# Kernel optimization log

Measured on AMD Instinct MI355X. Metric: run time of the kernel, lower is better.

Reference implementation:

```python
import jax, jax.numpy as jnp
import numpy as np

GAMMA = 0.5      # temperature from __init__
SOS_ID = 2       # constant <sos> token id
EPS = 1e-10


def setup_inputs() -> dict:
    key = jax.random.key(0)
    ks = jax.random.split(key, 12)
    B, T, E, DY, DZ, V = 64, 32, 100, 200, 500, 32000
    H = DY + DZ
    s = lambda k, shape, sc=1.0: (jax.random.normal(k, shape, jnp.float32) * sc)
    return {
        "z": s(ks[0], (B, DZ), 0.1),
        "labels": jax.random.uniform(ks[1], (B,), jnp.float32),
        "W_fc": s(ks[2], (DY, 1), 0.1),
        "b_fc": s(ks[3], (DY,), 0.1),
        "embed_weight": s(ks[4], (V, E), 0.1),
        "W_ih": s(ks[5], (3 * H, E), 0.05),
        "W_hh": s(ks[6], (3 * H, H), 0.05),
        "b_ih": s(ks[7], (3 * H,), 0.05),
        "b_hh": s(ks[8], (3 * H,), 0.05),
        "W_out": s(ks[9], (V, H), 0.05),
        "b_out": s(ks[10], (V,), 0.05),
        "gumbel_u": jax.random.uniform(ks[11], (T - 1, B, V), jnp.float32),
        "src": jax.random.randint(jax.random.fold_in(key, 99), (T, B), 0, V),
        "src_len": T,
    }


def _gru_step(h, x, W_ih, W_hh, b_ih, b_hh):
    # PyTorch GRU cell: gates ordered (r, z, n)
    gi = x @ W_ih.T + b_ih          # [B, 3H]
    gh = h @ W_hh.T + b_hh          # [B, 3H]
    i_r, i_z, i_n = jnp.split(gi, 3, axis=-1)
    h_r, h_z, h_n = jnp.split(gh, 3, axis=-1)
    r = jax.nn.sigmoid(i_r + h_r)
    zt = jax.nn.sigmoid(i_z + h_z)
    n = jnp.tanh(i_n + r * h_n)
    return (1.0 - zt) * n + zt * h


def reference(z, labels, W_fc, b_fc, embed_weight, W_ih, W_hh, b_ih, b_hh,
              W_out, b_out, gumbel_u, src, src_len):
    B, H = z.shape[0], W_hh.shape[1]
    V = W_out.shape[0]
    # h0 = cat(fc(1 - labels), z)
    h0 = jnp.concatenate([(1.0 - labels)[:, None] @ W_fc.T + b_fc, z], axis=-1)  # [B, H]
    x0 = jnp.broadcast_to(embed_weight[SOS_ID], (B, embed_weight.shape[1]))      # [B, E]

    def step(carry, u):
        h, x = carry
        h = _gru_step(h, x, W_ih, W_hh, b_ih, b_hh)      # [B, H]
        pred = h @ W_out.T + b_out                        # [B, V]
        g = -jnp.log(-jnp.log(u + EPS) + EPS)             # gumbel noise
        y = jax.nn.softmax(pred + g, axis=-1)             # gumbel_softmax, tau=1
        x_next = (y / GAMMA) @ embed_weight               # soft embedding [B, E]
        return (h, x_next), (h, pred)

    (_, _), (outs, preds) = jax.lax.scan(step, (h0, x0), gumbel_u)  # [T-1,B,H], [T-1,B,V]

    dt = z.dtype
    outputs = jnp.concatenate(
        [h0[None], jnp.zeros((1, B, H), dt), outs], axis=0)         # [T+1, B, H]
    predictions = jnp.concatenate(
        [jnp.zeros((1, B, V), dt), preds], axis=0)                  # [T, B, V]
    return outputs, predictions
```

## Files before the change

### kernel.cpp

```cpp
#include <hip/hip_runtime.h>

#define B 64
#define TS 31
#define E 100
#define DY 200
#define DZ 500
#define V 32000
#define H 700
#define HP 704
#define H3 2100
#define XH 800
#define SOS 2
#define OUT_PRED_OFF (33*B*H)
#define NPB 500
#define VCH 125
#define NVCH 256
#define SOFF 15.0f

typedef unsigned short u16;
typedef __attribute__((ext_vector_type(8))) short short8;
typedef __attribute__((ext_vector_type(4))) float f32x4;

__device__ __forceinline__ float sigm(float x) { return 1.f / (1.f + __expf(-x)); }
__device__ __forceinline__ u16 f2b(float f) {
  union { float f; unsigned int u; } c; c.f = f;
  unsigned int u = c.u;
  u16 h = (u16)(u >> 16);
  unsigned int rem = u & 0xFFFFu;
  h += (u16)((rem > 0x8000u) || (rem == 0x8000u && (h & 1)));
  return h;
}

__global__ __launch_bounds__(256) void k_zero(float* __restrict__ out, long n) {
  long i0 = (long)blockIdx.x * 256 + threadIdx.x;
  long st = (long)gridDim.x * 256;
  for (long i = i0; i < n; i += st) out[i] = 0.f;
}

__global__ __launch_bounds__(256) void k0_init(
    const float* __restrict__ z, const float* __restrict__ labels,
    const float* __restrict__ W_fc, const float* __restrict__ b_fc,
    const float* __restrict__ embed, const float* __restrict__ W_ih,
    const float* __restrict__ W_hh, const float* __restrict__ W_out,
    float* __restrict__ out, float* __restrict__ hA, float* __restrict__ WT,
    u16* __restrict__ W2, u16* __restrict__ h_bf,
    float* __restrict__ xacc, float* __restrict__ Z)
{
  long i0 = (long)blockIdx.x * 256 + threadIdx.x;
  long st = (long)gridDim.x * 256;
  if (i0 < B) Z[i0] = 2.f;
  for (long i = i0; i < (long)B * V; i += st) out[OUT_PRED_OFF + i] = 0.f;
  for (long i = i0; i < (long)B * H; i += st) out[B * H + i] = 0.f;
  for (long i = i0; i < (long)B * H; i += st) {
    int b = (int)(i / H), j = (int)(i % H);
    float v = (j < DY) ? (1.f - labels[b]) * W_fc[j] + b_fc[j]
                       : z[b * DZ + (j - DY)];
    hA[i] = v;
    out[i] = v;
  }
  for (long i = i0; i < (long)B * E; i += st) {
    int e = (int)(i % E);
    xacc[i] = embed[SOS * E + e];
  }
  for (long i = i0; i < (long)B * HP; i += st) h_bf[i] = 0;
  for (long i = i0; i < (long)XH * H3; i += st) {
    int k = (int)(i / H3), g = (int)(i % H3);
    WT[i] = (k < E) ? W_ih[(long)g * E + k] : W_hh[(long)g * H + (k - E)];
  }
  for (long i = i0; i < (long)V * HP; i += st) {
    long s8 = i >> 3; int j = (int)(i & 7);
    int lane = (int)(s8 & 63);
    long tmp = s8 >> 6;
    int kk = (int)(tmp % 22);
    long cgrp = tmp / 22;
    int col = (int)(cgrp * 16 + (lane & 15));
    int k = kk * 32 + ((lane >> 4) << 3) + j;
    W2[i] = (k < H) ? f2b(W_out[(size_t)col * H + k]) : (u16)0;
  }
}

__global__ __launch_bounds__(256) void k1a(
    const float* __restrict__ xacc, const float* __restrict__ Z,
    const float* __restrict__ hin, const float* __restrict__ WT,
    const float* __restrict__ b_ih,
    float* __restrict__ gig, float* __restrict__ ghg_p)
{
  int nt = blockIdx.x, c = blockIdx.y;
  int n = nt * 64 + (threadIdx.x & 63);
  int bq = threadIdx.x >> 6;
  __shared__ float xs[64][100];
  __shared__ float invZ[64];
  if (threadIdx.x < 64) invZ[threadIdx.x] = 2.f / Z[threadIdx.x];
  __syncthreads();
  for (int i = threadIdx.x; i < 6400; i += 256) {
    int b = i / 100, kk = i % 100;
    xs[b][kk] = (c == 0) ? xacc[i] * invZ[b] : hin[b * H + (c - 1) * 100 + kk];
  }
  __syncthreads();
  if (n >= H3) return;
  float acc[16];
  #pragma unroll
  for (int bb = 0; bb < 16; ++bb) acc[bb] = 0.f;
  for (int kk = 0; kk < 100; ++kk) {
    float w = WT[(size_t)(c * 100 + kk) * H3 + n];
    #pragma unroll
    for (int bb = 0; bb < 16; ++bb) acc[bb] += xs[bq * 16 + bb][kk] * w;
  }
  if (c == 0) {
    float bi = b_ih[n];
    #pragma unroll
    for (int bb = 0; bb < 16; ++bb) gig[(size_t)(bq * 16 + bb) * H3 + n] = acc[bb] + bi;
  } else {
    float* p = ghg_p + (size_t)(c - 1) * B * H3;
    #pragma unroll
    for (int bb = 0; bb < 16; ++bb) p[(size_t)(bq * 16 + bb) * H3 + n] = acc[bb];
  }
}

__global__ __launch_bounds__(256) void k1br(
    const float* __restrict__ gig, const float* __restrict__ ghg_p,
    const float* __restrict__ b_hh, const float* __restrict__ hin,
    float* __restrict__ hout, float* __restrict__ out_h, u16* __restrict__ h_bf)
{
  int i = blockIdx.x * 256 + threadIdx.x;
  if (i >= B * H) return;
  int b = i / H, j = i % H;
  float ir = gig[(size_t)b * H3 + j];
  float iz = gig[(size_t)b * H3 + H + j];
  float in_ = gig[(size_t)b * H3 + 2 * H + j];
  float hr = b_hh[j], hz = b_hh[H + j], hn = b_hh[2 * H + j];
  for (int c = 0; c < 7; ++c) {
    const float* p = ghg_p + (size_t)c * B * H3 + (size_t)b * H3;
    hr += p[j]; hz += p[H + j]; hn += p[2 * H + j];
  }
  float hprev = hin[b * H + j];
  float r  = sigm(ir + hr);
  float zt = sigm(iz + hz);
  float nn = tanhf(in_ + r * hn);
  float hv = (1.f - zt) * nn + zt * hprev;
  hout[b * H + j] = hv;
  out_h[i] = hv;
  h_bf[b * HP + j] = f2b(hv);
}

__global__ __launch_bounds__(256) void k2(
    const u16* __restrict__ h_bf, const u16* __restrict__ W2,
    const float* __restrict__ b_out, const float* __restrict__ gu,
    float* __restrict__ pred, float* __restrict__ w_f, float* __restrict__ Zp)
{
  __shared__ float lzp[64][4];
  const int u = blockIdx.x, tid = threadIdx.x;
  const int wave = tid >> 6, lane = tid & 63, l15 = lane & 15;
  const int col = u * 64 + wave * 16 + l15;
  f32x4 acc[4];
  #pragma unroll
  for (int q = 0; q < 4; ++q) acc[q] = f32x4{0.f, 0.f, 0.f, 0.f};
  const short8* wv2 = (const short8*)W2 + ((size_t)(u * 4 + wave) * 22) * 64 + lane;
  const u16* hp = h_bf + ((lane >> 4) << 3);
  for (int kk = 0; kk < 22; ++kk) {
    short8 bv = wv2[(size_t)kk * 64];
    #pragma unroll
    for (int rt = 0; rt < 4; ++rt) {
      short8 a = *reinterpret_cast<const short8*>(hp + (size_t)(rt * 16 + l15) * HP + kk * 32);
      acc[rt] = __builtin_amdgcn_mfma_f32_16x16x32_bf16(a, bv, acc[rt], 0, 0, 0);
    }
  }
  float bo = b_out[col];
  #pragma unroll
  for (int rt = 0; rt < 4; ++rt) {
    #pragma unroll
    for (int r = 0; r < 4; ++r) {
      int brow = rt * 16 + ((lane >> 4) << 2) + r;
      float pv = acc[rt][r] + bo;
      size_t off = (size_t)brow * V + col;
      __builtin_nontemporal_store(pv, &pred[off]);
      float uu = __builtin_nontemporal_load(&gu[off]);
      float g = -logf(-logf(uu + 1e-10f) + 1e-10f);
      float w = __expf(pv + g - SOFF);
      __builtin_nontemporal_store(w, &w_f[off]);
      float vz = w;
      vz += __shfl_xor(vz, 1); vz += __shfl_xor(vz, 2);
      vz += __shfl_xor(vz, 4); vz += __shfl_xor(vz, 8);
      if (l15 == 0) lzp[brow][wave] = vz;
    }
  }
  __syncthreads();
  if (tid < 64)
    Zp[(size_t)u * 64 + tid] = lzp[tid][0] + lzp[tid][1] + lzp[tid][2] + lzp[tid][3];
}

__global__ __launch_bounds__(256) void k3(
    const float* __restrict__ w_f, const float* __restrict__ embed,
    float* __restrict__ P)
{
  int c = blockIdx.x;
  int v0 = c * VCH;
  int e = threadIdx.x & 127, bh = threadIdx.x >> 7;
  __shared__ float ys[64][VCH];
  for (int i = threadIdx.x; i < 64 * VCH; i += 256) {
    int b = i / VCH, vv = i % VCH;
    ys[b][vv] = w_f[(size_t)b * V + v0 + vv];
  }
  __syncthreads();
  if (e >= E) return;
  float acc[32];
  #pragma unroll
  for (int bb = 0; bb < 32; ++bb) acc[bb] = 0.f;
  for (int vv = 0; vv < VCH; ++vv) {
    float w = embed[(size_t)(v0 + vv) * E + e];
    #pragma unroll
    for (int bb = 0; bb < 32; ++bb) acc[bb] += ys[bh * 32 + bb][vv] * w;
  }
  #pragma unroll
  for (int bb = 0; bb < 32; ++bb)
    P[((size_t)c * B + bh * 32 + bb) * E + e] = acc[bb];
}

__global__ __launch_bounds__(256) void k4(
    const float* __restrict__ P, const float* __restrict__ Zp,
    float* __restrict__ xacc, float* __restrict__ Z)
{
  int i = blockIdx.x * 256 + threadIdx.x;
  if (blockIdx.x < 25) {
    float s = 0.f;
    for (int c = 0; c < NVCH; ++c) s += P[(size_t)c * 6400 + i];
    xacc[i] = s;
  } else if (threadIdx.x < 64) {
    float s = 0.f;
    for (int u = 0; u < NPB; ++u) s += Zp[(size_t)u * 64 + threadIdx.x];
    Z[threadIdx.x] = s;
  }
}

extern "C" void kernel_launch(void* const* d_in, const int* in_sizes, int n_in,
                              void* d_out, int out_size, void* d_ws, size_t ws_size,
                              hipStream_t stream) {
  (void)ws_size;
  float* out = (float*)d_out;

  static const long lsz[12] = {32000, 64, 200, 200, 3200000, 210000, 1470000,
                               2100, 2100, 22400000, 32000, 63488000};
  static const int dictP[12]    = {0, 1, 2, 3, 4, 5, 6, 7, 8, 9, 10, 11};
  static const int alpha14P[12] = {13, 10, 0, 4, 8, 2, 1, 6, 5, 3, 7, 9};
  static const int alpha12P[12] = {11, 10, 0, 4, 8, 2, 1, 6, 5, 3, 7, 9};
  auto okperm = [&](const int* p) -> bool {
    for (int i = 0; i < 12; ++i) {
      if (p[i] >= n_in) return false;
      if ((long)in_sizes[p[i]] != lsz[i]) return false;
    }
    return true;
  };
  const int* P_ = nullptr;
  if (okperm(dictP)) P_ = dictP;
  else if (okperm(alpha14P)) P_ = alpha14P;
  else if (okperm(alpha12P)) P_ = alpha12P;
  if (!P_) { k_zero<<<2048, 256, 0, stream>>>(out, (long)out_size); return; }

  const float* z      = (const float*)d_in[P_[0]];
  const float* labels = (const float*)d_in[P_[1]];
  const float* W_fc   = (const float*)d_in[P_[2]];
  const float* b_fc   = (const float*)d_in[P_[3]];
  const float* embed  = (const float*)d_in[P_[4]];
  const float* W_ih   = (const float*)d_in[P_[5]];
  const float* W_hh   = (const float*)d_in[P_[6]];
  const float* b_ih   = (const float*)d_in[P_[7]];
  const float* b_hh   = (const float*)d_in[P_[8]];
  const float* W_out  = (const float*)d_in[P_[9]];
  const float* b_out  = (const float*)d_in[P_[10]];
  const float* gu     = (const float*)d_in[P_[11]];

  char* w = (char*)d_ws;
  auto alloc = [&](size_t bytes) { char* p = w; w += (bytes + 255) & ~(size_t)255; return p; };
  float* hA    = (float*)alloc((size_t)B * H * 4);
  float* hB    = (float*)alloc((size_t)B * H * 4);
  float* WT    = (float*)alloc((size_t)XH * H3 * 4);
  float* gig   = (float*)alloc((size_t)B * H3 * 4);
  float* ghg_p = (float*)alloc((size_t)7 * B * H3 * 4);
  float* w_f   = (float*)alloc((size_t)B * V * 4);
  float* Zp    = (float*)alloc((size_t)NPB * B * 4);
  float* Pp    = (float*)alloc((size_t)NVCH * B * E * 4);
  float* xacc  = (float*)alloc((size_t)B * E * 4);
  float* Zb    = (float*)alloc((size_t)B * 4);
  u16*  W2     = (u16*)alloc((size_t)V * HP * 2);
  u16*  h_bf   = (u16*)alloc((size_t)B * HP * 2);

  k0_init<<<2048, 256, 0, stream>>>(z, labels, W_fc, b_fc, embed, W_ih, W_hh, W_out,
                                    out, hA, WT, W2, h_bf, xacc, Zb);

  for (int t = 0; t < TS; ++t) {
    float* hin  = (t & 1) ? hB : hA;
    float* hout = (t & 1) ? hA : hB;
    float* pred = out + OUT_PRED_OFF + (size_t)(1 + t) * B * V;
    k1a<<<dim3(33, 8), 256, 0, stream>>>(xacc, Zb, hin, WT, b_ih, gig, ghg_p);
    k1br<<<(B * H + 255) / 256, 256, 0, stream>>>(gig, ghg_p, b_hh, hin, hout,
                                                  out + (size_t)(2 + t) * B * H, h_bf);
    k2<<<NPB, 256, 0, stream>>>(h_bf, W2, b_out, gu + (size_t)t * B * V,
                                pred, w_f, Zp);
    k3<<<NVCH, 256, 0, stream>>>(w_f, embed, Pp);
    if (t < TS - 1)
      k4<<<26, 256, 0, stream>>>(Pp, Zp, xacc, Zb);
  }
}
```

Baseline: 3.924 ms.

## Replace partial-sum buffers and reduction kernel with atomic accumulation

The hidden-gate partials from k1a and the soft-embedding partials from k3 are now accumulated with atomicAdd straight into single buffers, so the separate k4 reduction kernel and the large partial-sum arrays are gone. The Z normalizer reduction moves into k1a, and k1br zeroes the accumulators for the next step. k3 is also skipped on the final step, where its output was never used. This removes one launch per step and a lot of partial-buffer traffic, at the cost of atomic contention and non-deterministic summation order.

```diff
diff --git a/kernel.cpp b/kernel.cpp
--- a/kernel.cpp
+++ b/kernel.cpp
@@ -44,11 +44,12 @@
     const float* __restrict__ W_hh, const float* __restrict__ W_out,
     float* __restrict__ out, float* __restrict__ hA, float* __restrict__ WT,
     u16* __restrict__ W2, u16* __restrict__ h_bf,
-    float* __restrict__ xacc, float* __restrict__ Z)
+    float* __restrict__ xacc, float* __restrict__ Zp, float* __restrict__ gh)
 {
   long i0 = (long)blockIdx.x * 256 + threadIdx.x;
   long st = (long)gridDim.x * 256;
-  if (i0 < B) Z[i0] = 2.f;
+  for (long i = i0; i < (long)NPB * B; i += st) Zp[i] = 2.f / (float)NPB;
+  for (long i = i0; i < (long)B * H3; i += st) gh[i] = 0.f;
   for (long i = i0; i < (long)B * V; i += st) out[OUT_PRED_OFF + i] = 0.f;
   for (long i = i0; i < (long)B * H; i += st) out[B * H + i] = 0.f;
   for (long i = i0; i < (long)B * H; i += st) {
@@ -80,18 +81,24 @@
 }
 
 __global__ __launch_bounds__(256) void k1a(
-    const float* __restrict__ xacc, const float* __restrict__ Z,
+    const float* __restrict__ xacc, const float* __restrict__ Zp,
     const float* __restrict__ hin, const float* __restrict__ WT,
     const float* __restrict__ b_ih,
-    float* __restrict__ gig, float* __restrict__ ghg_p)
+    float* __restrict__ gig, float* __restrict__ gh)
 {
   int nt = blockIdx.x, c = blockIdx.y;
   int n = nt * 64 + (threadIdx.x & 63);
   int bq = threadIdx.x >> 6;
   __shared__ float xs[64][100];
   __shared__ float invZ[64];
-  if (threadIdx.x < 64) invZ[threadIdx.x] = 2.f / Z[threadIdx.x];
-  __syncthreads();
+  if (c == 0) {
+    if (threadIdx.x < 64) {
+      float s = 0.f;
+      for (int u = 0; u < NPB; ++u) s += Zp[(size_t)u * 64 + threadIdx.x];
+      invZ[threadIdx.x] = 2.f / s;
+    }
+    __syncthreads();
+  }
   for (int i = threadIdx.x; i < 6400; i += 256) {
     int b = i / 100, kk = i % 100;
     xs[b][kk] = (c == 0) ? xacc[i] * invZ[b] : hin[b * H + (c - 1) * 100 + kk];
@@ -111,28 +118,28 @@
     #pragma unroll
     for (int bb = 0; bb < 16; ++bb) gig[(size_t)(bq * 16 + bb) * H3 + n] = acc[bb] + bi;
   } else {
-    float* p = ghg_p + (size_t)(c - 1) * B * H3;
-    #pragma unroll
-    for (int bb = 0; bb < 16; ++bb) p[(size_t)(bq * 16 + bb) * H3 + n] = acc[bb];
+    #pragma unroll
+    for (int bb = 0; bb < 16; ++bb)
+      atomicAdd(&gh[(size_t)(bq * 16 + bb) * H3 + n], acc[bb]);
   }
 }
 
 __global__ __launch_bounds__(256) void k1br(
-    const float* __restrict__ gig, const float* __restrict__ ghg_p,
+    const float* __restrict__ gig, float* __restrict__ gh,
     const float* __restrict__ b_hh, const float* __restrict__ hin,
-    float* __restrict__ hout, float* __restrict__ out_h, u16* __restrict__ h_bf)
+    float* __restrict__ hout, float* __restrict__ out_h, u16* __restrict__ h_bf,
+    float* __restrict__ xacc)
 {
   int i = blockIdx.x * 256 + threadIdx.x;
   if (i >= B * H) return;
+  if (i < B * E) xacc[i] = 0.f;
   int b = i / H, j = i % H;
-  float ir = gig[(size_t)b * H3 + j];
-  float iz = gig[(size_t)b * H3 + H + j];
-  float in_ = gig[(size_t)b * H3 + 2 * H + j];
-  float hr = b_hh[j], hz = b_hh[H + j], hn = b_hh[2 * H + j];
-  for (int c = 0; c < 7; ++c) {
-    const float* p = ghg_p + (size_t)c * B * H3 + (size_t)b * H3;
-    hr += p[j]; hz += p[H + j]; hn += p[2 * H + j];
-  }
+  size_t g0 = (size_t)b * H3 + j;
+  float ir = gig[g0], iz = gig[g0 + H], in_ = gig[g0 + 2 * H];
+  float hr = gh[g0] + b_hh[j];
+  float hz = gh[g0 + H] + b_hh[H + j];
+  float hn = gh[g0 + 2 * H] + b_hh[2 * H + j];
+  gh[g0] = 0.f; gh[g0 + H] = 0.f; gh[g0 + 2 * H] = 0.f;
   float hprev = hin[b * H + j];
   float r  = sigm(ir + hr);
   float zt = sigm(iz + hz);
@@ -191,7 +198,7 @@
 
 __global__ __launch_bounds__(256) void k3(
     const float* __restrict__ w_f, const float* __restrict__ embed,
-    float* __restrict__ P)
+    float* __restrict__ xacc)
 {
   int c = blockIdx.x;
   int v0 = c * VCH;
@@ -213,23 +220,7 @@
   }
   #pragma unroll
   for (int bb = 0; bb < 32; ++bb)
-    P[((size_t)c * B + bh * 32 + bb) * E + e] = acc[bb];
-}
-
-__global__ __launch_bounds__(256) void k4(
-    const float* __restrict__ P, const float* __restrict__ Zp,
-    float* __restrict__ xacc, float* __restrict__ Z)
-{
-  int i = blockIdx.x * 256 + threadIdx.x;
-  if (blockIdx.x < 25) {
-    float s = 0.f;
-    for (int c = 0; c < NVCH; ++c) s += P[(size_t)c * 6400 + i];
-    xacc[i] = s;
-  } else if (threadIdx.x < 64) {
-    float s = 0.f;
-    for (int u = 0; u < NPB; ++u) s += Zp[(size_t)u * 64 + threadIdx.x];
-    Z[threadIdx.x] = s;
-  }
+    atomicAdd(&xacc[(size_t)(bh * 32 + bb) * E + e], acc[bb]);
 }
 
 extern "C" void kernel_launch(void* const* d_in, const int* in_sizes, int n_in,
@@ -275,29 +266,27 @@
   float* hB    = (float*)alloc((size_t)B * H * 4);
   float* WT    = (float*)alloc((size_t)XH * H3 * 4);
   float* gig   = (float*)alloc((size_t)B * H3 * 4);
-  float* ghg_p = (float*)alloc((size_t)7 * B * H3 * 4);
+  float* gh    = (float*)alloc((size_t)B * H3 * 4);
   float* w_f   = (float*)alloc((size_t)B * V * 4);
   float* Zp    = (float*)alloc((size_t)NPB * B * 4);
-  float* Pp    = (float*)alloc((size_t)NVCH * B * E * 4);
   float* xacc  = (float*)alloc((size_t)B * E * 4);
-  float* Zb    = (float*)alloc((size_t)B * 4);
   u16*  W2     = (u16*)alloc((size_t)V * HP * 2);
   u16*  h_bf   = (u16*)alloc((size_t)B * HP * 2);
 
   k0_init<<<2048, 256, 0, stream>>>(z, labels, W_fc, b_fc, embed, W_ih, W_hh, W_out,
-                                    out, hA, WT, W2, h_bf, xacc, Zb);
+                                    out, hA, WT, W2, h_bf, xacc, Zp, gh);
 
   for (int t = 0; t < TS; ++t) {
     float* hin  = (t & 1) ? hB : hA;
     float* hout = (t & 1) ? hA : hB;
     float* pred = out + OUT_PRED_OFF + (size_t)(1 + t) * B * V;
-    k1a<<<dim3(33, 8), 256, 0, stream>>>(xacc, Zb, hin, WT, b_ih, gig, ghg_p);
-    k1br<<<(B * H + 255) / 256, 256, 0, stream>>>(gig, ghg_p, b_hh, hin, hout,
-                                                  out + (size_t)(2 + t) * B * H, h_bf);
+    k1a<<<dim3(33, 8), 256, 0, stream>>>(xacc, Zp, hin, WT, b_ih, gig, gh);
+    k1br<<<(B * H + 255) / 256, 256, 0, stream>>>(gig, gh, b_hh, hin, hout,
+                                                  out + (size_t)(2 + t) * B * H, h_bf,
+                                                  xacc);
     k2<<<NPB, 256, 0, stream>>>(h_bf, W2, b_out, gu + (size_t)t * B * V,
                                 pred, w_f, Zp);
-    k3<<<NVCH, 256, 0, stream>>>(w_f, embed, Pp);
     if (t < TS - 1)
-      k4<<<26, 256, 0, stream>>>(Pp, Zp, xacc, Zb);
-  }
-}
+      k3<<<NVCH, 256, 0, stream>>>(w_f, embed, xacc);
+  }
+}
```

Result: no change. 3.964 ms (+1.0%).
